# Kernel tuning notes

Hardware: AMD Instinct MI355X
Metric: run time of the kernel (lower is better)

Reference implementation:

```python
import jax, jax.numpy as jnp
import numpy as np

NEG = -1000000000.0

def setup_inputs() -> dict:
    key = jax.random.key(0)
    k1, k2, k3, k4, k5, k6 = jax.random.split(key, 6)
    B, T, H = 32, 4096, 512
    scale = 1.0 / np.sqrt(H)
    return {
        "enc_seq": jax.random.normal(k1, (B, T, H), dtype=jnp.float32),
        "enc_mask": jax.random.randint(k2, (B, T), 0, 2, dtype=jnp.int32),
        "dec_state": jax.random.normal(k3, (B, H), dtype=jnp.float32),
        "W_h": jax.random.normal(k4, (H, H), dtype=jnp.float32) * scale,
        "W_s": jax.random.normal(k5, (H, H), dtype=jnp.float32) * scale,
        "v": jax.random.normal(k6, (H,), dtype=jnp.float32) * scale,
    }

def reference(enc_seq, enc_mask, dec_state, W_h, W_s, v):
    # torch nn.Linear computes x @ W.T; weights here stored as (out, in) = (H, H)
    h = jnp.einsum("bth,oh->bto", enc_seq, W_h)          # [B,T,H]
    s = jnp.einsum("bh,oh->bo", dec_state, W_s)[:, None]  # [B,1,H]
    e = jnp.einsum("bth,h->bt", jnp.tanh(h + s), v)       # [B,T]
    e = jnp.where(enc_mask == 0, NEG, e)
    a = jax.nn.softmax(e, axis=1)                          # [B,T]
    ctx = jnp.einsum("bt,bth->bh", a, enc_seq)             # [B,H]
    return ctx
```

## Files before the change

kernel.cpp:

```cpp
#include <hip/hip_runtime.h>
#include <hip/hip_bf16.h>

#define B_ 32
#define T_ 4096
#define H_ 512
#define NEGV (-1000000000.0f)

using bf16x8  = __attribute__((ext_vector_type(8))) __bf16;
using short8  = __attribute__((ext_vector_type(8))) short;
using f32x4   = __attribute__((ext_vector_type(4))) float;

static __device__ __forceinline__ short f2bf(float f) {
    unsigned u = __builtin_bit_cast(unsigned, f);
    unsigned r = (u + 0x7fffu + ((u >> 16) & 1u)) >> 16;
    return (short)r;
}

static __device__ __forceinline__ float tanh_fast(float x) {
    float e = __builtin_amdgcn_exp2f(x * 2.8853900817779268f);
    return 1.0f - 2.0f * __builtin_amdgcn_rcpf(e + 1.0f);
}

static __device__ __forceinline__ f32x4 mfma16(short8 a, short8 b, f32x4 c) {
    return __builtin_amdgcn_mfma_f32_16x16x32_bf16(
        __builtin_bit_cast(bf16x8, a), __builtin_bit_cast(bf16x8, b), c, 0, 0, 0);
}

#define GLOAD_LDS16(g, l)                                                     \
    __builtin_amdgcn_global_load_lds(                                         \
        (const __attribute__((address_space(1))) unsigned*)(g),               \
        (__attribute__((address_space(3))) unsigned*)(l), 16, 0, 0)

__global__ __launch_bounds__(256) void wh_prep(const float* __restrict__ Wh,
                                               short* __restrict__ Whp) {
    int id = blockIdx.x * 256 + threadIdx.x;
    int n = id >> 6, kc = id & 63;
    const float4* src = (const float4*)(Wh + (size_t)n * H_ + kc * 8);
    float4 f0 = src[0];
    float4 f1 = src[1];
    short8 t;
    t[0] = f2bf(f0.x); t[1] = f2bf(f0.y); t[2] = f2bf(f0.z); t[3] = f2bf(f0.w);
    t[4] = f2bf(f1.x); t[5] = f2bf(f1.y); t[6] = f2bf(f1.z); t[7] = f2bf(f1.w);
    int nc = n >> 5, r = n & 31;
    *(short8*)(Whp + nc * 16384 + r * 512 + ((kc ^ (n & 7)) << 3)) = t;
}

__global__ __launch_bounds__(256) void s_kernel(const float* __restrict__ dec,
                                                const float* __restrict__ Ws,
                                                float* __restrict__ s_out) {
    __shared__ float dec_l[H_];
    int b = blockIdx.y;
    int tid = threadIdx.x;
    dec_l[tid]       = dec[b * H_ + tid];
    dec_l[tid + 256] = dec[b * H_ + tid + 256];
    __syncthreads();
    int o = blockIdx.x * 256 + tid;
    const float4* w = (const float4*)(Ws + (size_t)o * H_);
    float acc = 0.f;
#pragma unroll 8
    for (int k = 0; k < H_ / 4; ++k) {
        float4 wv = w[k];
        acc += wv.x * dec_l[4 * k] + wv.y * dec_l[4 * k + 1] +
               wv.z * dec_l[4 * k + 2] + wv.w * dec_l[4 * k + 3];
    }
    s_out[b * H_ + o] = acc;
}

__global__ __launch_bounds__(256, 2) void e_kernel(const float* __restrict__ enc,
                                                   const int* __restrict__ mask,
                                                   const short* __restrict__ Whp,
                                                   const float* __restrict__ s_in,
                                                   const float* __restrict__ v,
                                                   float* __restrict__ e_out) {
    __shared__ short lds_b[2][32 * 512];
    __shared__ float s_l[H_];
    __shared__ float v_l[H_];

    const int tid  = threadIdx.x;
    const int wave = tid >> 6;
    const int lane = tid & 63;
    const int q    = lane >> 4;
    const int lq   = lane & 15;
    const int key  = lq & 7;

    const int row0 = blockIdx.x * 128;
    const int b    = row0 / T_;

    for (int i = tid; i < H_; i += 256) {
        s_l[i] = s_in[b * H_ + i];
        v_l[i] = v[i];
    }

    short8 afrag[2][16];
#pragma unroll
    for (int g = 0; g < 2; ++g) {
        int m = row0 + wave * 32 + g * 16 + lq;
        const float* ap = enc + (size_t)m * H_ + q * 8;
#pragma unroll
        for (int ks = 0; ks < 16; ++ks) {
            float4 f0 = *(const float4*)(ap + ks * 32);
            float4 f1 = *(const float4*)(ap + ks * 32 + 4);
            short8 t;
            t[0] = f2bf(f0.x); t[1] = f2bf(f0.y); t[2] = f2bf(f0.z); t[3] = f2bf(f0.w);
            t[4] = f2bf(f1.x); t[5] = f2bf(f1.y); t[6] = f2bf(f1.z); t[7] = f2bf(f1.w);
            afrag[g][ks] = t;
        }
    }

    {
        const char* gsrc = (const char*)Whp;
#pragma unroll
        for (int j = 0; j < 8; ++j) {
            int off = wave * 8192 + j * 1024;
            GLOAD_LDS16(gsrc + off + lane * 16, (char*)lds_b[0] + off);
        }
    }

    float e_acc[2][4] = {};
    __syncthreads();

    for (int nt = 0; nt < 16; ++nt) {
        if (nt < 15) {
            const char* gsrc = (const char*)Whp + (nt + 1) * 32768;
            short* dst = lds_b[(nt + 1) & 1];
#pragma unroll
            for (int j = 0; j < 8; ++j) {
                int off = wave * 8192 + j * 1024;
                GLOAD_LDS16(gsrc + off + lane * 16, (char*)dst + off);
            }
        }
        const short* cur = lds_b[nt & 1];
#pragma unroll
        for (int s = 0; s < 2; ++s) {
            const short* rowp = cur + (s * 16 + lq) * 512;
            f32x4 acc0 = {0.f, 0.f, 0.f, 0.f};
            f32x4 acc1 = {0.f, 0.f, 0.f, 0.f};
#pragma unroll
            for (int ks = 0; ks < 16; ++ks) {
                short8 bf = *(const short8*)(rowp + (((ks * 4 + q) ^ key) << 3));
                acc0 = mfma16(afrag[0][ks], bf, acc0);
                acc1 = mfma16(afrag[1][ks], bf, acc1);
            }
            int n = nt * 32 + s * 16 + lq;
            float sv = s_l[n];
            float vv = v_l[n];
#pragma unroll
            for (int r = 0; r < 4; ++r) {
                e_acc[0][r] += tanh_fast(acc0[r] + sv) * vv;
                e_acc[1][r] += tanh_fast(acc1[r] + sv) * vv;
            }
        }
        __syncthreads();
    }

#pragma unroll
    for (int g = 0; g < 2; ++g)
#pragma unroll
        for (int r = 0; r < 4; ++r) {
            float t = e_acc[g][r];
            t += __shfl_xor(t, 1, 16);
            t += __shfl_xor(t, 2, 16);
            t += __shfl_xor(t, 4, 16);
            t += __shfl_xor(t, 8, 16);
            if (lq == 0) {
                int m = row0 + wave * 32 + g * 16 + q * 4 + r;
                e_out[m] = mask[m] ? t : NEGV;
            }
        }
}

__global__ __launch_bounds__(256) void softmax_kernel(float* __restrict__ e) {
    __shared__ float red[256];
    int b = blockIdx.x, tid = threadIdx.x;
    float* eb = e + (size_t)b * T_;
    float m = -3.4e38f;
    for (int i = tid; i < T_; i += 256) m = fmaxf(m, eb[i]);
    red[tid] = m;
    __syncthreads();
    for (int s = 128; s > 0; s >>= 1) {
        if (tid < s) red[tid] = fmaxf(red[tid], red[tid + s]);
        __syncthreads();
    }
    m = red[0];
    __syncthreads();
    float sum = 0.f;
    for (int i = tid; i < T_; i += 256) {
        float p = __builtin_amdgcn_exp2f((eb[i] - m) * 1.4426950408889634f);
        eb[i] = p;
        sum += p;
    }
    red[tid] = sum;
    __syncthreads();
    for (int s = 128; s > 0; s >>= 1) {
        if (tid < s) red[tid] += red[tid + s];
        __syncthreads();
    }
    float inv = 1.0f / red[0];
    for (int i = tid; i < T_; i += 256) eb[i] *= inv;
}

__global__ __launch_bounds__(256) void ctx_kernel(const float* __restrict__ enc,
                                                  const float* __restrict__ a,
                                                  float* __restrict__ out) {
    constexpr int TC = 128;
    __shared__ float a_l[TC];
    int b = blockIdx.y, tc = blockIdx.x;
    int tid = threadIdx.x;
    int t0 = tc * TC;
    if (tid < TC) a_l[tid] = a[(size_t)b * T_ + t0 + tid];
    __syncthreads();
    const float2* ep = (const float2*)(enc + ((size_t)b * T_ + t0) * H_) + tid;
    float2 acc = {0.f, 0.f};
#pragma unroll 8
    for (int t = 0; t < TC; ++t) {
        float2 v2 = ep[(size_t)t * (H_ / 2)];
        float w = a_l[t];
        acc.x += w * v2.x;
        acc.y += w * v2.y;
    }
    atomicAdd(&out[b * H_ + 2 * tid], acc.x);
    atomicAdd(&out[b * H_ + 2 * tid + 1], acc.y);
}

extern "C" void kernel_launch(void* const* d_in, const int* in_sizes, int n_in,
                              void* d_out, int out_size, void* d_ws, size_t ws_size,
                              hipStream_t stream) {
    (void)in_sizes; (void)n_in; (void)ws_size;
    const float* enc  = (const float*)d_in[0];
    const int*   mask = (const int*)d_in[1];
    const float* dec  = (const float*)d_in[2];
    const float* Wh   = (const float*)d_in[3];
    const float* Ws   = (const float*)d_in[4];
    const float* v    = (const float*)d_in[5];
    float* out = (float*)d_out;

    short* whp_buf = (short*)d_ws;
    float* s_buf   = (float*)(whp_buf + 512 * 512);
    float* e_buf   = s_buf + B_ * H_;

    wh_prep<<<dim3(128), 256, 0, stream>>>(Wh, whp_buf);
    s_kernel<<<dim3(2, B_), 256, 0, stream>>>(dec, Ws, s_buf);
    e_kernel<<<dim3(B_ * T_ / 128), 256, 0, stream>>>(enc, mask, whp_buf, s_buf, v, e_buf);
    softmax_kernel<<<dim3(B_), 256, 0, stream>>>(e_buf);
    hipMemsetAsync(d_out, 0, (size_t)out_size * sizeof(float), stream);
    ctx_kernel<<<dim3(T_ / 128, B_), 256, 0, stream>>>(enc, e_buf, out);
}
```

Measured before the change: 508.6 us.

## Halve e_kernel W tile for occupancy, shuffle softmax, two-stage ctx reduction

The e_kernel now streams 16-row W_h tiles instead of 32-row tiles, which halves its LDS footprint, and raises the launch bound to three blocks per CU. The s and v vectors are packed into one float2 LDS array. Softmax now runs with 1024 threads, keeps values in registers and reduces with wave shuffles. The ctx atomics and memset are replaced by a partial-sum stage followed by a small reduction kernel. The cost is more loop iterations and barriers in e_kernel and register pressure from the higher occupancy target, which may cause spills with 32 afrag registers.

```diff
diff --git a/kernel.cpp b/kernel.cpp
--- a/kernel.cpp
+++ b/kernel.cpp
@@ -41,8 +41,7 @@
     short8 t;
     t[0] = f2bf(f0.x); t[1] = f2bf(f0.y); t[2] = f2bf(f0.z); t[3] = f2bf(f0.w);
     t[4] = f2bf(f1.x); t[5] = f2bf(f1.y); t[6] = f2bf(f1.z); t[7] = f2bf(f1.w);
-    int nc = n >> 5, r = n & 31;
-    *(short8*)(Whp + nc * 16384 + r * 512 + ((kc ^ (n & 7)) << 3)) = t;
+    *(short8*)(Whp + (n >> 4) * 8192 + (n & 15) * 512 + ((kc ^ (n & 7)) << 3)) = t;
 }
 
 __global__ __launch_bounds__(256) void s_kernel(const float* __restrict__ dec,
@@ -66,15 +65,14 @@
     s_out[b * H_ + o] = acc;
 }
 
-__global__ __launch_bounds__(256, 2) void e_kernel(const float* __restrict__ enc,
+__global__ __launch_bounds__(256, 3) void e_kernel(const float* __restrict__ enc,
                                                    const int* __restrict__ mask,
                                                    const short* __restrict__ Whp,
                                                    const float* __restrict__ s_in,
                                                    const float* __restrict__ v,
                                                    float* __restrict__ e_out) {
-    __shared__ short lds_b[2][32 * 512];
-    __shared__ float s_l[H_];
-    __shared__ float v_l[H_];
+    __shared__ short lds_b[2][16 * 512];
+    __shared__ float2 sv_l[H_];
 
     const int tid  = threadIdx.x;
     const int wave = tid >> 6;
@@ -86,10 +84,8 @@
     const int row0 = blockIdx.x * 128;
     const int b    = row0 / T_;
 
-    for (int i = tid; i < H_; i += 256) {
-        s_l[i] = s_in[b * H_ + i];
-        v_l[i] = v[i];
-    }
+    for (int i = tid; i < H_; i += 256)
+        sv_l[i] = make_float2(s_in[b * H_ + i], v[i]);
 
     short8 afrag[2][16];
 #pragma unroll
@@ -107,48 +103,39 @@
         }
     }
 
-    {
-        const char* gsrc = (const char*)Whp;
-#pragma unroll
-        for (int j = 0; j < 8; ++j) {
-            int off = wave * 8192 + j * 1024;
-            GLOAD_LDS16(gsrc + off + lane * 16, (char*)lds_b[0] + off);
-        }
+#pragma unroll
+    for (int j = 0; j < 4; ++j) {
+        int off = wave * 4096 + j * 1024;
+        GLOAD_LDS16((const char*)Whp + off + lane * 16, (char*)lds_b[0] + off);
     }
 
     float e_acc[2][4] = {};
     __syncthreads();
 
-    for (int nt = 0; nt < 16; ++nt) {
-        if (nt < 15) {
-            const char* gsrc = (const char*)Whp + (nt + 1) * 32768;
-            short* dst = lds_b[(nt + 1) & 1];
-#pragma unroll
-            for (int j = 0; j < 8; ++j) {
-                int off = wave * 8192 + j * 1024;
-                GLOAD_LDS16(gsrc + off + lane * 16, (char*)dst + off);
+    for (int nt = 0; nt < 32; ++nt) {
+        if (nt < 31) {
+            const char* gsrc = (const char*)Whp + (nt + 1) * 16384;
+            char* dst = (char*)lds_b[(nt + 1) & 1];
+#pragma unroll
+            for (int j = 0; j < 4; ++j) {
+                int off = wave * 4096 + j * 1024;
+                GLOAD_LDS16(gsrc + off + lane * 16, dst + off);
             }
         }
-        const short* cur = lds_b[nt & 1];
-#pragma unroll
-        for (int s = 0; s < 2; ++s) {
-            const short* rowp = cur + (s * 16 + lq) * 512;
-            f32x4 acc0 = {0.f, 0.f, 0.f, 0.f};
-            f32x4 acc1 = {0.f, 0.f, 0.f, 0.f};
-#pragma unroll
-            for (int ks = 0; ks < 16; ++ks) {
-                short8 bf = *(const short8*)(rowp + (((ks * 4 + q) ^ key) << 3));
-                acc0 = mfma16(afrag[0][ks], bf, acc0);
-                acc1 = mfma16(afrag[1][ks], bf, acc1);
-            }
-            int n = nt * 32 + s * 16 + lq;
-            float sv = s_l[n];
-            float vv = v_l[n];
-#pragma unroll
-            for (int r = 0; r < 4; ++r) {
-                e_acc[0][r] += tanh_fast(acc0[r] + sv) * vv;
-                e_acc[1][r] += tanh_fast(acc1[r] + sv) * vv;
-            }
+        const short* rowp = lds_b[nt & 1] + lq * 512;
+        f32x4 acc0 = {0.f, 0.f, 0.f, 0.f};
+        f32x4 acc1 = {0.f, 0.f, 0.f, 0.f};
+#pragma unroll
+        for (int ks = 0; ks < 16; ++ks) {
+            short8 bf = *(const short8*)(rowp + (((ks * 4 + q) ^ key) << 3));
+            acc0 = mfma16(afrag[0][ks], bf, acc0);
+            acc1 = mfma16(afrag[1][ks], bf, acc1);
+        }
+        float2 sv = sv_l[nt * 16 + lq];
+#pragma unroll
+        for (int r = 0; r < 4; ++r) {
+            e_acc[0][r] += tanh_fast(acc0[r] + sv.x) * sv.y;
+            e_acc[1][r] += tanh_fast(acc1[r] + sv.x) * sv.y;
         }
         __syncthreads();
     }
@@ -169,63 +156,80 @@
         }
 }
 
-__global__ __launch_bounds__(256) void softmax_kernel(float* __restrict__ e) {
-    __shared__ float red[256];
+__global__ __launch_bounds__(1024) void softmax_kernel(float* __restrict__ e) {
+    __shared__ float red[16];
     int b = blockIdx.x, tid = threadIdx.x;
+    int wid = tid >> 6, lane = tid & 63;
     float* eb = e + (size_t)b * T_;
-    float m = -3.4e38f;
-    for (int i = tid; i < T_; i += 256) m = fmaxf(m, eb[i]);
-    red[tid] = m;
-    __syncthreads();
-    for (int s = 128; s > 0; s >>= 1) {
-        if (tid < s) red[tid] = fmaxf(red[tid], red[tid + s]);
-        __syncthreads();
-    }
+    float4 x = *(float4*)(eb + tid * 4);
+
+    float m = fmaxf(fmaxf(x.x, x.y), fmaxf(x.z, x.w));
+#pragma unroll
+    for (int s = 1; s < 64; s <<= 1) m = fmaxf(m, __shfl_xor(m, s, 64));
+    if (lane == 0) red[wid] = m;
+    __syncthreads();
     m = red[0];
-    __syncthreads();
-    float sum = 0.f;
-    for (int i = tid; i < T_; i += 256) {
-        float p = __builtin_amdgcn_exp2f((eb[i] - m) * 1.4426950408889634f);
-        eb[i] = p;
-        sum += p;
-    }
-    red[tid] = sum;
-    __syncthreads();
-    for (int s = 128; s > 0; s >>= 1) {
-        if (tid < s) red[tid] += red[tid + s];
-        __syncthreads();
-    }
-    float inv = 1.0f / red[0];
-    for (int i = tid; i < T_; i += 256) eb[i] *= inv;
-}
-
-__global__ __launch_bounds__(256) void ctx_kernel(const float* __restrict__ enc,
+#pragma unroll
+    for (int j = 1; j < 16; ++j) m = fmaxf(m, red[j]);
+    __syncthreads();
+
+    const float L2E = 1.4426950408889634f;
+    x.x = __builtin_amdgcn_exp2f((x.x - m) * L2E);
+    x.y = __builtin_amdgcn_exp2f((x.y - m) * L2E);
+    x.z = __builtin_amdgcn_exp2f((x.z - m) * L2E);
+    x.w = __builtin_amdgcn_exp2f((x.w - m) * L2E);
+    float sum = x.x + x.y + x.z + x.w;
+#pragma unroll
+    for (int s = 1; s < 64; s <<= 1) sum += __shfl_xor(sum, s, 64);
+    if (lane == 0) red[wid] = sum;
+    __syncthreads();
+    sum = 0.f;
+#pragma unroll
+    for (int j = 0; j < 16; ++j) sum += red[j];
+
+    float inv = 1.0f / sum;
+    x.x *= inv; x.y *= inv; x.z *= inv; x.w *= inv;
+    *(float4*)(eb + tid * 4) = x;
+}
+
+__global__ __launch_bounds__(256) void ctx_stage1(const float* __restrict__ enc,
                                                   const float* __restrict__ a,
-                                                  float* __restrict__ out) {
-    constexpr int TC = 128;
+                                                  float* __restrict__ part) {
+    constexpr int TC = 256;
     __shared__ float a_l[TC];
     int b = blockIdx.y, tc = blockIdx.x;
     int tid = threadIdx.x;
     int t0 = tc * TC;
-    if (tid < TC) a_l[tid] = a[(size_t)b * T_ + t0 + tid];
-    __syncthreads();
-    const float2* ep = (const float2*)(enc + ((size_t)b * T_ + t0) * H_) + tid;
-    float2 acc = {0.f, 0.f};
+    a_l[tid] = a[(size_t)b * T_ + t0 + tid];
+    __syncthreads();
+    int hq = tid & 127, tpar = tid >> 7;
+    const float4* ep = (const float4*)(enc + ((size_t)b * T_ + t0) * H_) + hq;
+    float4 acc = {0.f, 0.f, 0.f, 0.f};
 #pragma unroll 8
-    for (int t = 0; t < TC; ++t) {
-        float2 v2 = ep[(size_t)t * (H_ / 2)];
+    for (int t = tpar; t < TC; t += 2) {
+        float4 v4 = ep[(size_t)t * (H_ / 4)];
         float w = a_l[t];
-        acc.x += w * v2.x;
-        acc.y += w * v2.y;
-    }
-    atomicAdd(&out[b * H_ + 2 * tid], acc.x);
-    atomicAdd(&out[b * H_ + 2 * tid + 1], acc.y);
+        acc.x += w * v4.x; acc.y += w * v4.y;
+        acc.z += w * v4.z; acc.w += w * v4.w;
+    }
+    float4* pp = (float4*)(part + ((size_t)(b * 32 + tc * 2 + tpar)) * H_) + hq;
+    *pp = acc;
+}
+
+__global__ __launch_bounds__(512) void ctx_stage2(const float* __restrict__ part,
+                                                  float* __restrict__ out) {
+    int b = blockIdx.x, h = threadIdx.x;
+    const float* p = part + (size_t)b * 32 * H_ + h;
+    float acc = 0.f;
+#pragma unroll
+    for (int j = 0; j < 32; ++j) acc += p[j * H_];
+    out[b * H_ + h] = acc;
 }
 
 extern "C" void kernel_launch(void* const* d_in, const int* in_sizes, int n_in,
                               void* d_out, int out_size, void* d_ws, size_t ws_size,
                               hipStream_t stream) {
-    (void)in_sizes; (void)n_in; (void)ws_size;
+    (void)in_sizes; (void)n_in; (void)ws_size; (void)out_size;
     const float* enc  = (const float*)d_in[0];
     const int*   mask = (const int*)d_in[1];
     const float* dec  = (const float*)d_in[2];
@@ -237,11 +241,12 @@
     short* whp_buf = (short*)d_ws;
     float* s_buf   = (float*)(whp_buf + 512 * 512);
     float* e_buf   = s_buf + B_ * H_;
+    float* part    = e_buf + B_ * T_;
 
     wh_prep<<<dim3(128), 256, 0, stream>>>(Wh, whp_buf);
     s_kernel<<<dim3(2, B_), 256, 0, stream>>>(dec, Ws, s_buf);
     e_kernel<<<dim3(B_ * T_ / 128), 256, 0, stream>>>(enc, mask, whp_buf, s_buf, v, e_buf);
-    softmax_kernel<<<dim3(B_), 256, 0, stream>>>(e_buf);
-    hipMemsetAsync(d_out, 0, (size_t)out_size * sizeof(float), stream);
-    ctx_kernel<<<dim3(T_ / 128, B_), 256, 0, stream>>>(enc, e_buf, out);
-}
+    softmax_kernel<<<dim3(B_), 1024, 0, stream>>>(e_buf);
+    ctx_stage1<<<dim3(T_ / 256, B_), 256, 0, stream>>>(enc, e_buf, part);
+    ctx_stage2<<<dim3(B_), 512, 0, stream>>>(part, out);
+}
```

Measured after the change: 580.6 us. 1.14x slower.
